# Kernel optimization log

Hardware: AMD Instinct MI355X
Metric: run time of the kernel (lower is better)

Reference implementation:

```python
import jax, jax.numpy as jnp
import numpy as np

CH = 64
SCALE = 2
GROUPS = 4
K = 3
GN_GROUPS = min(CH // 8, 8)  # = 8
EPS_GN = 1e-5
EPS_COS = 1e-8


def setup_inputs() -> dict:
    key = jax.random.key(0)
    ks = jax.random.split(key, 4)
    B, H, W = 8, 256, 256
    OC = 2 * GROUPS
    lap = jnp.array([[0., -1., 0.], [-1., 4., -1.], [0., -1., 0.]], dtype=jnp.float32)
    hp_weight = jnp.tile(lap[None, None], (CH, 1, 1, 1))  # depthwise high-pass kernel
    return {
        "x": jax.random.normal(ks[0], (B, CH, H, W), dtype=jnp.float32),
        "gn_gamma": jnp.ones((CH,), jnp.float32),
        "gn_beta": jnp.zeros((CH,), jnp.float32),
        "hp_weight": hp_weight,
        "dir_w": jax.random.normal(ks[1], (OC, K * K - 1), jnp.float32) * 0.001,
        "dir_b": jnp.zeros((OC,), jnp.float32),
        "mag_w": jax.random.normal(ks[2], (OC, CH), jnp.float32) * 0.02,
        "mag_b": jnp.zeros((OC,), jnp.float32),
        "hfg_w": jax.random.normal(ks[3], (OC, CH), jnp.float32) * 0.02,
        "hfg_b": jnp.zeros((OC,), jnp.float32),
    }


def group_norm(x, gamma, beta, g, eps=EPS_GN):
    B, C, H, W = x.shape
    xr = x.reshape(B, g, -1)
    mu = xr.mean(-1, keepdims=True)
    var = xr.var(-1, keepdims=True)
    xn = ((xr - mu) * jax.lax.rsqrt(var + eps)).reshape(B, C, H, W)
    return xn * gamma[None, :, None, None] + beta[None, :, None, None]


def dw_conv3(x, w):
    # depthwise 3x3, padding=1, no bias
    return jax.lax.conv_general_dilated(
        x, w, window_strides=(1, 1), padding=((1, 1), (1, 1)),
        dimension_numbers=("NCHW", "OIHW", "NCHW"), feature_group_count=x.shape[1])


def avg_pool(x, s):
    B, C, H, W = x.shape
    return x.reshape(B, C, H // s, s, W // s, s).mean(axis=(3, 5))


def direction_feat(x, k=K):
    # cosine similarity (over channels) of center pixel vs each of k*k neighbors, center dropped
    B, C, H, W = x.shape
    p = k // 2
    xp = jnp.pad(x, ((0, 0), (0, 0), (p, p), (p, p)))
    patches = jnp.stack([xp[:, :, i:i + H, j:j + W]
                         for i in range(k) for j in range(k)], axis=2)  # [B,C,k2,H,W]
    center = patches[:, :, k * k // 2:k * k // 2 + 1]  # [B,C,1,H,W]
    dot = (center * patches).sum(axis=1)               # [B,k2,H,W]
    n1 = jnp.sqrt((center * center).sum(axis=1))       # [B,1,H,W]
    n2 = jnp.sqrt((patches * patches).sum(axis=1))     # [B,k2,H,W]
    sim = dot / (jnp.maximum(n1, EPS_COS) * jnp.maximum(n2, EPS_COS))
    c = k * k // 2
    return jnp.concatenate([sim[:, :c], sim[:, c + 1:]], axis=1)  # [B,k2-1,H,W]


def conv1x1(w, b, x):
    return jnp.einsum("oc,bchw->bohw", w, x) + b[None, :, None, None]


def grid_sample_border(x, grid):
    # x: [N,C,H,W]; grid: [N,Hg,Wg,2] in [-1,1]; bilinear, align_corners=False, padding_mode='border'
    N, C, H, W = x.shape
    gx, gy = grid[..., 0], grid[..., 1]
    ix = jnp.clip(((gx + 1.0) * W - 1.0) * 0.5, 0.0, W - 1.0)
    iy = jnp.clip(((gy + 1.0) * H - 1.0) * 0.5, 0.0, H - 1.0)
    x0 = jnp.floor(ix); y0 = jnp.floor(iy)
    wx = (ix - x0)[..., None]; wy = (iy - y0)[..., None]
    x0i = jnp.clip(x0.astype(jnp.int32), 0, W - 1)
    y0i = jnp.clip(y0.astype(jnp.int32), 0, H - 1)
    x1i = jnp.clip(x0i + 1, 0, W - 1)
    y1i = jnp.clip(y0i + 1, 0, H - 1)
    img = x.transpose(0, 2, 3, 1)  # [N,H,W,C]
    b = jnp.arange(N)[:, None, None]
    v00 = img[b, y0i, x0i]; v01 = img[b, y0i, x1i]
    v10 = img[b, y1i, x0i]; v11 = img[b, y1i, x1i]
    out = (v00 * (1 - wx) * (1 - wy) + v01 * wx * (1 - wy)
           + v10 * (1 - wx) * wy + v11 * wx * wy)
    return out.transpose(0, 3, 1, 2)  # [N,C,Hg,Wg]


def reference(x, gn_gamma, gn_beta, hp_weight, dir_w, dir_b, mag_w, mag_b, hfg_w, hfg_b):
    B, C, H, W = x.shape
    xn = group_norm(x, gn_gamma, gn_beta, GN_GROUPS)
    hf = dw_conv3(xn, hp_weight)
    xl = avg_pool(xn, SCALE)
    hfl = avg_pool(hf, SCALE)
    df = direction_feat(xl)
    gate = jax.nn.sigmoid(conv1x1(mag_w, mag_b, xl) + conv1x1(hfg_w, hfg_b, hfl))
    offset = conv1x1(dir_w, dir_b, df) * gate  # [B, 2*GROUPS, Hl, Wl]
    Hl, Wl = H // SCALE, W // SCALE
    off = offset.reshape(B, 2, GROUPS, Hl, Wl)
    cy = jnp.arange(Hl, dtype=x.dtype) * SCALE + SCALE / 2.0  # high-res pixel centers
    cx = jnp.arange(Wl, dtype=x.dtype) * SCALE + SCALE / 2.0
    gx = (cx[None, None, None, :] + off[:, 0]) * (2.0 / W) - 1.0  # [B,G,Hl,Wl]
    gy = (cy[None, None, :, None] + off[:, 1]) * (2.0 / H) - 1.0
    grid = jnp.stack([gx, gy], axis=-1).reshape(B * GROUPS, Hl, Wl, 2)
    xg = x.reshape(B * GROUPS, C // GROUPS, H, W)
    out = grid_sample_border(xg, grid)
    return out.reshape(B, C, Hl, Wl)
```

## Files before the change

### kernel.cpp

```cpp
#include <hip/hip_runtime.h>
#include <hip/hip_bf16.h>
#include <math.h>

#define B_ 8
#define C_ 64
#define H_ 256
#define W_ 256
#define HL_ 128
#define WL_ 128
#define GN_G 8
#define CPG 8
#define GRP 4
#define OC_ 8
#define GROUP_ELEMS (CPG * H_ * W_)

#define TILE_H 16
#define XROWS 34
#define EOW 132

__device__ __forceinline__ float bf2f(unsigned short u) {
  return __uint_as_float(((unsigned)u) << 16);
}

__global__ __launch_bounds__(256) void k2_fused(const float* __restrict__ x,
                                                const float* __restrict__ hpw,
                                                __hip_bfloat16* __restrict__ px,
                                                __hip_bfloat16* __restrict__ pL,
                                                float* __restrict__ partials) {
  __shared__ float E[XROWS][EOW];
  __shared__ float O[XROWS][EOW];
  __shared__ float rs[4], rs2[4];
  const int t = threadIdx.x;
  const int blk = blockIdx.x;
  const int tileIdx = blk & 7;
  const int bc = blk >> 3;
  const int c = bc & 63;
  const int hl0 = tileIdx * TILE_H;
  const float* plane = x + (size_t)bc * (H_ * W_);
  const int y0 = 2 * hl0 - 1;

  if (t < XROWS * 2) {
    const int r = t >> 1;
    if (t & 1) E[r][128] = 0.f; else O[r][0] = 0.f;
  }

  float s = 0.f, s2 = 0.f;
  for (int i = 0; i < 9; ++i) {
    const int q = t + i * 256;
    if (q >= XROWS * 64) break;
    const int r = q >> 6;
    const int k = q & 63;
    const int y = y0 + r;
    float4 v = make_float4(0.f, 0.f, 0.f, 0.f);
    if ((unsigned)y < (unsigned)H_)
      v = *reinterpret_cast<const float4*>(plane + y * W_ + (k << 2));
    E[r][2 * k]     = v.x;
    E[r][2 * k + 1] = v.z;
    O[r][2 * k + 1] = v.y;
    O[r][2 * k + 2] = v.w;
    if (r >= 1 && r <= 32) {
      s  += v.x + v.y + v.z + v.w;
      s2 += v.x * v.x + v.y * v.y + v.z * v.z + v.w * v.w;
    }
  }
#pragma unroll
  for (int off = 32; off > 0; off >>= 1) {
    s  += __shfl_down(s, off, 64);
    s2 += __shfl_down(s2, off, 64);
  }
  if ((t & 63) == 0) { rs[t >> 6] = s; rs2[t >> 6] = s2; }
  __syncthreads();
  if (t == 0) {
    partials[blk * 2 + 0] = rs[0] + rs[1] + rs[2] + rs[3];
    partials[blk * 2 + 1] = rs2[0] + rs2[1] + rs2[2] + rs2[3];
  }

  float w[9];
#pragma unroll
  for (int i = 0; i < 9; ++i) w[i] = hpw[c * 9 + i];

  const int wl = t & 127;
  const int hs = (t >> 7) * 8;
  const int rbase = 2 * hs;
  float win[4][4];
#pragma unroll
  for (int j = 0; j < 4; ++j) {
    win[j][0] = O[rbase + j][wl];
    win[j][1] = E[rbase + j][wl];
    win[j][2] = O[rbase + j][wl + 1];
    win[j][3] = E[rbase + j][wl + 1];
  }

  int outIdx = (bc * HL_ + (hl0 + hs)) * WL_ + wl;
#pragma unroll
  for (int i = 0; i < 8; ++i) {
    float pr[4][3];
#pragma unroll
    for (int j = 0; j < 4; ++j)
#pragma unroll
      for (int d = 0; d < 3; ++d) pr[j][d] = win[j][d] + win[j][d + 1];
    float hfsum = 0.f;
    float q11 = 0.f;
#pragma unroll
    for (int j = 0; j < 3; ++j)
#pragma unroll
      for (int d = 0; d < 3; ++d) {
        const float qq = pr[j][d] + pr[j + 1][d];
        hfsum = fmaf(w[j * 3 + d], qq, hfsum);
        if (j == 1 && d == 1) q11 = qq;
      }
    px[outIdx] = __float2bfloat16(0.25f * q11);
    pL[outIdx] = __float2bfloat16(0.25f * hfsum);
    outIdx += WL_;
    if (i < 7) {
      const int rn = rbase + 2 * i + 4;
#pragma unroll
      for (int d = 0; d < 4; ++d) {
        win[0][d] = win[2][d];
        win[1][d] = win[3][d];
      }
      win[2][0] = O[rn][wl];     win[2][1] = E[rn][wl];
      win[2][2] = O[rn][wl + 1]; win[2][3] = E[rn][wl + 1];
      win[3][0] = O[rn + 1][wl];     win[3][1] = E[rn + 1][wl];
      win[3][2] = O[rn + 1][wl + 1]; win[3][3] = E[rn + 1][wl + 1];
    }
  }
}

#define TS 16
__global__ __launch_bounds__(256) void k34_fused(const float* __restrict__ x,
                                                 const __hip_bfloat16* __restrict__ px,
                                                 const __hip_bfloat16* __restrict__ pL,
                                                 const float* __restrict__ partials,
                                                 const float* __restrict__ gamma,
                                                 const float* __restrict__ beta,
                                                 const float* __restrict__ dir_w,
                                                 const float* __restrict__ dir_b,
                                                 const float* __restrict__ mag_w,
                                                 const float* __restrict__ mag_b,
                                                 const float* __restrict__ hfg_w,
                                                 const float* __restrict__ hfg_b,
                                                 float* __restrict__ out) {
  __shared__ float s_v[2][16][18][24];
  __shared__ float s_mw[C_][OC_];
  __shared__ float s_hw[C_][OC_];
  __shared__ float s_dir[OC_][8];
  __shared__ float s_ab2[C_][2];
  __shared__ float s_bias[2][OC_];

  const int tid = threadIdx.x;
  const int bx = blockIdx.x;
  const int tx = bx & 7, ty = (bx >> 3) & 7, b = bx >> 6;
  const int hl0 = ty * TS, wl0 = tx * TS;
  const size_t planeSz = (size_t)HL_ * WL_;

  for (int i = tid; i < OC_ * C_; i += 256) {
    const int o = i >> 6, c = i & 63;
    s_mw[c][o] = mag_w[i];
    s_hw[c][o] = hfg_w[i];
  }
  if (tid < 64) s_dir[tid >> 3][tid & 7] = dir_w[tid];
  if (tid < OC_) { s_bias[0][tid] = mag_b[tid] + hfg_b[tid]; s_bias[1][tid] = dir_b[tid]; }
  if (tid < 64) {
    const int c = tid, g = c >> 3;
    float S = 0.f, S2 = 0.f;
    for (int c2 = g * CPG; c2 < g * CPG + CPG; ++c2)
#pragma unroll
      for (int p2 = 0; p2 < 8; ++p2) {
        const int blk2 = (b * 64 + c2) * 8 + p2;
        S  += partials[blk2 * 2 + 0];
        S2 += partials[blk2 * 2 + 1];
      }
    const float N = (float)GROUP_ELEMS;
    const float mean = S / N;
    const float var = fmaxf(S2 / N - mean * mean, 0.f);
    const float a = rsqrtf(var + 1e-5f) * gamma[c];
    s_ab2[c][0] = a;
    s_ab2[c][1] = beta[c] - mean * a;
  }
  __syncthreads();

  auto stage = [&](int cc, int sel) {
    for (int q = tid; q < 16 * 18 * 6; q += 256) {
      const int c = q / 108, rem = q % 108, r = rem / 6, f4 = rem % 6;
      const int cg = cc * 16 + c;
      const int gy = hl0 - 1 + r;
      const int gx0 = wl0 - 4 + f4 * 4;
      const float a = s_ab2[cg][0], bb = s_ab2[cg][1];
      const __hip_bfloat16* pp = px + (size_t)(b * C_ + cg) * planeSz + gy * WL_ + gx0;
      float4 v = make_float4(0.f, 0.f, 0.f, 0.f);
      if ((unsigned)gy < (unsigned)HL_) {
        if (gx0 >= 0 && gx0 + 3 < WL_) {
          const ushort4 rv = *reinterpret_cast<const ushort4*>(pp);
          v.x = fmaf(a, bf2f(rv.x), bb); v.y = fmaf(a, bf2f(rv.y), bb);
          v.z = fmaf(a, bf2f(rv.z), bb); v.w = fmaf(a, bf2f(rv.w), bb);
        } else {
          const unsigned short* ps = reinterpret_cast<const unsigned short*>(pp);
          if ((unsigned)(gx0 + 0) < (unsigned)WL_) v.x = fmaf(a, bf2f(ps[0]), bb);
          if ((unsigned)(gx0 + 1) < (unsigned)WL_) v.y = fmaf(a, bf2f(ps[1]), bb);
          if ((unsigned)(gx0 + 2) < (unsigned)WL_) v.z = fmaf(a, bf2f(ps[2]), bb);
          if ((unsigned)(gx0 + 3) < (unsigned)WL_) v.w = fmaf(a, bf2f(ps[3]), bb);
        }
      }
      *reinterpret_cast<float4*>(&s_v[sel][c][r][f4 * 4]) = v;
    }
  };

  const int pxi = tid & 15, pyi = tid >> 4;
  const int hl = hl0 + pyi, wl = wl0 + pxi;
  const float mterm = 0.5f * ((hl == 0) + (hl == HL_ - 1) + (wl == 0) + (wl == WL_ - 1));

  float dot[8], n2[8], z[8], n1 = 0.f;
#pragma unroll
  for (int k = 0; k < 8; ++k) { dot[k] = 0.f; n2[k] = 0.f; z[k] = 0.f; }

  stage(0, 0);
  __syncthreads();

  for (int cc = 0; cc < 4; ++cc) {
    if (cc < 3) stage(cc + 1, (cc + 1) & 1);
    const int sel = cc & 1;
    float lh[16];
    {
      const unsigned short* lp = reinterpret_cast<const unsigned short*>(
          pL + (size_t)(b * C_ + cc * 16) * planeSz + hl * WL_ + wl);
#pragma unroll
      for (int c = 0; c < 16; ++c) lh[c] = bf2f(lp[c * planeSz]);
    }
#pragma unroll
    for (int c = 0; c < 16; ++c) {
      const int cg = cc * 16 + c;
      const float a = s_ab2[cg][0], bb = s_ab2[cg][1];
      const float vc = s_v[sel][c][pyi + 1][pxi + 4];
      const float vh = fmaf(a, lh[c], bb * mterm);
      n1 = fmaf(vc, vc, n1);
      const float u0 = s_v[sel][c][pyi][pxi + 3];
      const float u1 = s_v[sel][c][pyi][pxi + 4];
      const float u2 = s_v[sel][c][pyi][pxi + 5];
      const float u3 = s_v[sel][c][pyi + 1][pxi + 3];
      const float u4 = s_v[sel][c][pyi + 1][pxi + 5];
      const float u5 = s_v[sel][c][pyi + 2][pxi + 3];
      const float u6 = s_v[sel][c][pyi + 2][pxi + 4];
      const float u7 = s_v[sel][c][pyi + 2][pxi + 5];
      dot[0] = fmaf(vc, u0, dot[0]); n2[0] = fmaf(u0, u0, n2[0]);
      dot[1] = fmaf(vc, u1, dot[1]); n2[1] = fmaf(u1, u1, n2[1]);
      dot[2] = fmaf(vc, u2, dot[2]); n2[2] = fmaf(u2, u2, n2[2]);
      dot[3] = fmaf(vc, u3, dot[3]); n2[3] = fmaf(u3, u3, n2[3]);
      dot[4] = fmaf(vc, u4, dot[4]); n2[4] = fmaf(u4, u4, n2[4]);
      dot[5] = fmaf(vc, u5, dot[5]); n2[5] = fmaf(u5, u5, n2[5]);
      dot[6] = fmaf(vc, u6, dot[6]); n2[6] = fmaf(u6, u6, n2[6]);
      dot[7] = fmaf(vc, u7, dot[7]); n2[7] = fmaf(u7, u7, n2[7]);
      const float4 mw0 = *reinterpret_cast<const float4*>(&s_mw[cg][0]);
      const float4 mw1 = *reinterpret_cast<const float4*>(&s_mw[cg][4]);
      const float4 hw0 = *reinterpret_cast<const float4*>(&s_hw[cg][0]);
      const float4 hw1 = *reinterpret_cast<const float4*>(&s_hw[cg][4]);
      z[0] = fmaf(mw0.x, vc, fmaf(hw0.x, vh, z[0]));
      z[1] = fmaf(mw0.y, vc, fmaf(hw0.y, vh, z[1]));
      z[2] = fmaf(mw0.z, vc, fmaf(hw0.z, vh, z[2]));
      z[3] = fmaf(mw0.w, vc, fmaf(hw0.w, vh, z[3]));
      z[4] = fmaf(mw1.x, vc, fmaf(hw1.x, vh, z[4]));
      z[5] = fmaf(mw1.y, vc, fmaf(hw1.y, vh, z[5]));
      z[6] = fmaf(mw1.z, vc, fmaf(hw1.z, vh, z[6]));
      z[7] = fmaf(mw1.w, vc, fmaf(hw1.w, vh, z[7]));
    }
    __syncthreads();
  }

  const float n1c = fmaxf(sqrtf(n1), 1e-8f);
  float df[8];
#pragma unroll
  for (int k = 0; k < 8; ++k)
    df[k] = dot[k] / (n1c * fmaxf(sqrtf(n2[k]), 1e-8f));

  float off[8];
#pragma unroll
  for (int o = 0; o < 8; ++o) {
    float t1 = s_bias[1][o];
#pragma unroll
    for (int j = 0; j < 8; ++j) t1 = fmaf(s_dir[o][j], df[j], t1);
    const float zz = z[o] + s_bias[0][o];
    off[o] = t1 / (1.f + expf(-zz));
  }

  const float* planeB = x + (size_t)(b * C_) * (H_ * W_);
  float* outB = out + (size_t)(b * C_) * planeSz + hl * WL_ + wl;
#pragma unroll
  for (int g = 0; g < GRP; ++g) {
    const float ix = fminf(fmaxf(2.f * wl + 0.5f + off[g], 0.f), (float)(W_ - 1));
    const float iy = fminf(fmaxf(2.f * hl + 0.5f + off[GRP + g], 0.f), (float)(H_ - 1));
    const float x0f = floorf(ix), y0f = floorf(iy);
    const float wx = ix - x0f, wy = iy - y0f;
    const int x0 = (int)x0f, y0 = (int)y0f;
    const float w00 = (1.f - wx) * (1.f - wy), w01 = wx * (1.f - wy);
    const float w10 = (1.f - wx) * wy,        w11 = wx * wy;
    const float* pc = planeB + (size_t)(g * 16) * (H_ * W_);
    float* oc = outB + (size_t)(g * 16) * planeSz;
    if (__builtin_expect(((x0 | y0) & 1) == 0, 1)) {
#pragma unroll 4
      for (int c2 = 0; c2 < 16; ++c2) {
        const float2 r0 = *reinterpret_cast<const float2*>(pc + y0 * W_ + x0);
        const float2 r1 = *reinterpret_cast<const float2*>(pc + (y0 + 1) * W_ + x0);
        *oc = fmaf(r0.x, w00, fmaf(r0.y, w01, fmaf(r1.x, w10, r1.y * w11)));
        pc += H_ * W_;
        oc += planeSz;
      }
    } else {
      const int x1 = min(x0 + 1, W_ - 1), y1 = min(y0 + 1, H_ - 1);
#pragma unroll 4
      for (int c2 = 0; c2 < 16; ++c2) {
        const float v00 = pc[y0 * W_ + x0];
        const float v01 = pc[y0 * W_ + x1];
        const float v10 = pc[y1 * W_ + x0];
        const float v11 = pc[y1 * W_ + x1];
        *oc = fmaf(v00, w00, fmaf(v01, w01, fmaf(v10, w10, v11 * w11)));
        pc += H_ * W_;
        oc += planeSz;
      }
    }
  }
}

extern "C" void kernel_launch(void* const* d_in, const int* in_sizes, int n_in,
                              void* d_out, int out_size, void* d_ws, size_t ws_size,
                              hipStream_t stream) {
  const float* x = (const float*)d_in[0];
  const float* gn_gamma = (const float*)d_in[1];
  const float* gn_beta = (const float*)d_in[2];
  const float* hp_weight = (const float*)d_in[3];
  const float* dir_w = (const float*)d_in[4];
  const float* dir_b = (const float*)d_in[5];
  const float* mag_w = (const float*)d_in[6];
  const float* mag_b = (const float*)d_in[7];
  const float* hfg_w = (const float*)d_in[8];
  const float* hfg_b = (const float*)d_in[9];
  float* out = (float*)d_out;

  float* ws = (float*)d_ws;
  float* partials = ws;
  __hip_bfloat16* px = (__hip_bfloat16*)(ws + 8192);
  __hip_bfloat16* pL = px + (size_t)B_ * C_ * HL_ * WL_;

  k2_fused<<<B_ * C_ * 8, 256, 0, stream>>>(x, hp_weight, px, pL, partials);
  k34_fused<<<B_ * (HL_ / TS) * (WL_ / TS), 256, 0, stream>>>(
      x, px, pL, partials, gn_gamma, gn_beta, dir_w, dir_b,
      mag_w, mag_b, hfg_w, hfg_b, out);
}
```

Before: 89.66 us.

## Split channel reduction across thread pairs with smaller 8x16 tiles in k34

The k34 kernel now uses 8x16 output tiles, doubling the grid to 1024 blocks. Each pixel is handled by two threads that take alternating channels and combine their partial dot, norm and gate sums with a lane-xor shuffle. The offsets are shared through LDS so the bilinear sampling is split across both threads by group pairs. Shared memory drops and the double-buffered staging is replaced with single-buffer staging behind two barriers per chunk, which trades lost overlap and larger halo overhead for more parallelism and occupancy.

New measurement: 95.56 us. 1.07x slower.

```diff
diff --git a/kernel.cpp b/kernel.cpp
--- a/kernel.cpp
+++ b/kernel.cpp
@@ -127,7 +127,6 @@
   }
 }
 
-#define TS 16
 __global__ __launch_bounds__(256) void k34_fused(const float* __restrict__ x,
                                                  const __hip_bfloat16* __restrict__ px,
                                                  const __hip_bfloat16* __restrict__ pL,
@@ -141,7 +140,7 @@
                                                  const float* __restrict__ hfg_w,
                                                  const float* __restrict__ hfg_b,
                                                  float* __restrict__ out) {
-  __shared__ float s_v[2][16][18][24];
+  __shared__ float s_v[16][10][24];
   __shared__ float s_mw[C_][OC_];
   __shared__ float s_hw[C_][OC_];
   __shared__ float s_dir[OC_][8];
@@ -150,8 +149,8 @@
 
   const int tid = threadIdx.x;
   const int bx = blockIdx.x;
-  const int tx = bx & 7, ty = (bx >> 3) & 7, b = bx >> 6;
-  const int hl0 = ty * TS, wl0 = tx * TS;
+  const int tx = bx & 7, ty = (bx >> 3) & 15, b = bx >> 7;
+  const int hl0 = ty * 8, wl0 = tx * 16;
   const size_t planeSz = (size_t)HL_ * WL_;
 
   for (int i = tid; i < OC_ * C_; i += 256) {
@@ -178,16 +177,37 @@
     s_ab2[c][0] = a;
     s_ab2[c][1] = beta[c] - mean * a;
   }
-  __syncthreads();
-
-  auto stage = [&](int cc, int sel) {
-    for (int q = tid; q < 16 * 18 * 6; q += 256) {
-      const int c = q / 108, rem = q % 108, r = rem / 6, f4 = rem % 6;
-      const int cg = cc * 16 + c;
+
+  const int cg = tid & 1, pix = tid >> 1;
+  const int pxi = pix & 15, pyi = pix >> 4;
+  const int hl = hl0 + pyi, wl = wl0 + pxi;
+  const float mterm = 0.5f * ((hl == 0) + (hl == HL_ - 1) + (wl == 0) + (wl == WL_ - 1));
+
+  float dot[8], n2[8], z[8], n1 = 0.f;
+#pragma unroll
+  for (int k = 0; k < 8; ++k) { dot[k] = 0.f; n2[k] = 0.f; z[k] = 0.f; }
+
+  for (int cc = 0; cc < 4; ++cc) {
+    float lh[8];
+    {
+      const unsigned short* lp = reinterpret_cast<const unsigned short*>(
+          pL + (size_t)(b * C_ + cc * 16 + cg) * planeSz + hl * WL_ + wl);
+#pragma unroll
+      for (int j = 0; j < 8; ++j) lh[j] = bf2f(lp[2 * j * planeSz]);
+    }
+
+    __syncthreads();
+
+    for (int q = tid; q < 960; q += 256) {
+      const int c = q / 60;
+      const int rem = q - c * 60;
+      const int r = rem / 6;
+      const int f4 = rem - r * 6;
+      const int cgl = cc * 16 + c;
       const int gy = hl0 - 1 + r;
       const int gx0 = wl0 - 4 + f4 * 4;
-      const float a = s_ab2[cg][0], bb = s_ab2[cg][1];
-      const __hip_bfloat16* pp = px + (size_t)(b * C_ + cg) * planeSz + gy * WL_ + gx0;
+      const float a = s_ab2[cgl][0], bb = s_ab2[cgl][1];
+      const __hip_bfloat16* pp = px + (size_t)(b * C_ + cgl) * planeSz + gy * WL_ + gx0;
       float4 v = make_float4(0.f, 0.f, 0.f, 0.f);
       if ((unsigned)gy < (unsigned)HL_) {
         if (gx0 >= 0 && gx0 + 3 < WL_) {
@@ -202,46 +222,26 @@
           if ((unsigned)(gx0 + 3) < (unsigned)WL_) v.w = fmaf(a, bf2f(ps[3]), bb);
         }
       }
-      *reinterpret_cast<float4*>(&s_v[sel][c][r][f4 * 4]) = v;
-    }
-  };
-
-  const int pxi = tid & 15, pyi = tid >> 4;
-  const int hl = hl0 + pyi, wl = wl0 + pxi;
-  const float mterm = 0.5f * ((hl == 0) + (hl == HL_ - 1) + (wl == 0) + (wl == WL_ - 1));
-
-  float dot[8], n2[8], z[8], n1 = 0.f;
-#pragma unroll
-  for (int k = 0; k < 8; ++k) { dot[k] = 0.f; n2[k] = 0.f; z[k] = 0.f; }
-
-  stage(0, 0);
-  __syncthreads();
-
-  for (int cc = 0; cc < 4; ++cc) {
-    if (cc < 3) stage(cc + 1, (cc + 1) & 1);
-    const int sel = cc & 1;
-    float lh[16];
-    {
-      const unsigned short* lp = reinterpret_cast<const unsigned short*>(
-          pL + (size_t)(b * C_ + cc * 16) * planeSz + hl * WL_ + wl);
-#pragma unroll
-      for (int c = 0; c < 16; ++c) lh[c] = bf2f(lp[c * planeSz]);
-    }
-#pragma unroll
-    for (int c = 0; c < 16; ++c) {
-      const int cg = cc * 16 + c;
-      const float a = s_ab2[cg][0], bb = s_ab2[cg][1];
-      const float vc = s_v[sel][c][pyi + 1][pxi + 4];
-      const float vh = fmaf(a, lh[c], bb * mterm);
+      *reinterpret_cast<float4*>(&s_v[c][r][f4 * 4]) = v;
+    }
+    __syncthreads();
+
+#pragma unroll
+    for (int j = 0; j < 8; ++j) {
+      const int cl = 2 * j + cg;
+      const int cgl = cc * 16 + cl;
+      const float a = s_ab2[cgl][0], bb = s_ab2[cgl][1];
+      const float vc = s_v[cl][pyi + 1][pxi + 4];
+      const float vh = fmaf(a, lh[j], bb * mterm);
       n1 = fmaf(vc, vc, n1);
-      const float u0 = s_v[sel][c][pyi][pxi + 3];
-      const float u1 = s_v[sel][c][pyi][pxi + 4];
-      const float u2 = s_v[sel][c][pyi][pxi + 5];
-      const float u3 = s_v[sel][c][pyi + 1][pxi + 3];
-      const float u4 = s_v[sel][c][pyi + 1][pxi + 5];
-      const float u5 = s_v[sel][c][pyi + 2][pxi + 3];
-      const float u6 = s_v[sel][c][pyi + 2][pxi + 4];
-      const float u7 = s_v[sel][c][pyi + 2][pxi + 5];
+      const float u0 = s_v[cl][pyi][pxi + 3];
+      const float u1 = s_v[cl][pyi][pxi + 4];
+      const float u2 = s_v[cl][pyi][pxi + 5];
+      const float u3 = s_v[cl][pyi + 1][pxi + 3];
+      const float u4 = s_v[cl][pyi + 1][pxi + 5];
+      const float u5 = s_v[cl][pyi + 2][pxi + 3];
+      const float u6 = s_v[cl][pyi + 2][pxi + 4];
+      const float u7 = s_v[cl][pyi + 2][pxi + 5];
       dot[0] = fmaf(vc, u0, dot[0]); n2[0] = fmaf(u0, u0, n2[0]);
       dot[1] = fmaf(vc, u1, dot[1]); n2[1] = fmaf(u1, u1, n2[1]);
       dot[2] = fmaf(vc, u2, dot[2]); n2[2] = fmaf(u2, u2, n2[2]);
@@ -250,10 +250,10 @@
       dot[5] = fmaf(vc, u5, dot[5]); n2[5] = fmaf(u5, u5, n2[5]);
       dot[6] = fmaf(vc, u6, dot[6]); n2[6] = fmaf(u6, u6, n2[6]);
       dot[7] = fmaf(vc, u7, dot[7]); n2[7] = fmaf(u7, u7, n2[7]);
-      const float4 mw0 = *reinterpret_cast<const float4*>(&s_mw[cg][0]);
-      const float4 mw1 = *reinterpret_cast<const float4*>(&s_mw[cg][4]);
-      const float4 hw0 = *reinterpret_cast<const float4*>(&s_hw[cg][0]);
-      const float4 hw1 = *reinterpret_cast<const float4*>(&s_hw[cg][4]);
+      const float4 mw0 = *reinterpret_cast<const float4*>(&s_mw[cgl][0]);
+      const float4 mw1 = *reinterpret_cast<const float4*>(&s_mw[cgl][4]);
+      const float4 hw0 = *reinterpret_cast<const float4*>(&s_hw[cgl][0]);
+      const float4 hw1 = *reinterpret_cast<const float4*>(&s_hw[cgl][4]);
       z[0] = fmaf(mw0.x, vc, fmaf(hw0.x, vh, z[0]));
       z[1] = fmaf(mw0.y, vc, fmaf(hw0.y, vh, z[1]));
       z[2] = fmaf(mw0.z, vc, fmaf(hw0.z, vh, z[2]));
@@ -263,8 +263,15 @@
       z[6] = fmaf(mw1.z, vc, fmaf(hw1.z, vh, z[6]));
       z[7] = fmaf(mw1.w, vc, fmaf(hw1.w, vh, z[7]));
     }
-    __syncthreads();
-  }
+  }
+
+#pragma unroll
+  for (int k = 0; k < 8; ++k) {
+    dot[k] += __shfl_xor(dot[k], 1);
+    n2[k]  += __shfl_xor(n2[k], 1);
+    z[k]   += __shfl_xor(z[k], 1);
+  }
+  n1 += __shfl_xor(n1, 1);
 
   const float n1c = fmaxf(sqrtf(n1), 1e-8f);
   float df[8];
@@ -282,12 +289,25 @@
     off[o] = t1 / (1.f + expf(-zz));
   }
 
+  __syncthreads();
+  float (*s_off)[128] = reinterpret_cast<float (*)[128]>(&s_v[0][0][0]);
+  if (cg == 0) {
+#pragma unroll
+    for (int o = 0; o < 8; ++o) s_off[o][pix] = off[o];
+  }
+  __syncthreads();
+
+  const int p = tid & 127, h = tid >> 7;
+  const int spxi = p & 15, spyi = p >> 4;
+  const int shl = hl0 + spyi, swl = wl0 + spxi;
   const float* planeB = x + (size_t)(b * C_) * (H_ * W_);
-  float* outB = out + (size_t)(b * C_) * planeSz + hl * WL_ + wl;
-#pragma unroll
-  for (int g = 0; g < GRP; ++g) {
-    const float ix = fminf(fmaxf(2.f * wl + 0.5f + off[g], 0.f), (float)(W_ - 1));
-    const float iy = fminf(fmaxf(2.f * hl + 0.5f + off[GRP + g], 0.f), (float)(H_ - 1));
+  float* outB = out + (size_t)(b * C_) * planeSz + shl * WL_ + swl;
+#pragma unroll
+  for (int gg = 0; gg < 2; ++gg) {
+    const int g = 2 * h + gg;
+    const float offx = s_off[g][p], offy = s_off[g + 4][p];
+    const float ix = fminf(fmaxf(2.f * swl + 0.5f + offx, 0.f), (float)(W_ - 1));
+    const float iy = fminf(fmaxf(2.f * shl + 0.5f + offy, 0.f), (float)(H_ - 1));
     const float x0f = floorf(ix), y0f = floorf(iy);
     const float wx = ix - x0f, wy = iy - y0f;
     const int x0 = (int)x0f, y0 = (int)y0f;
@@ -341,7 +361,7 @@
   __hip_bfloat16* pL = px + (size_t)B_ * C_ * HL_ * WL_;
 
   k2_fused<<<B_ * C_ * 8, 256, 0, stream>>>(x, hp_weight, px, pL, partials);
-  k34_fused<<<B_ * (HL_ / TS) * (WL_ / TS), 256, 0, stream>>>(
+  k34_fused<<<B_ * (HL_ / 8) * (WL_ / 16), 256, 0, stream>>>(
       x, px, pL, partials, gn_gamma, gn_beta, dir_w, dir_b,
       mag_w, mag_b, hfg_w, hfg_b, out);
 }
```
